# Optimization experiments

Hardware: AMD Instinct MI355X
Metric: run time of the kernel (lower is better)

## Reference

```python
import jax, jax.numpy as jnp
import numpy as np

S, B, E, H, M = 1024, 4, 1024, 16, 128  # seq, batch, embed, heads, model_dims (key width)
V = E // H                              # value_dims = 64
_WSCALE = 1.0 / np.sqrt(E)              # keep softmax logits O(1)


def _cplx(re, im):
    return jax.lax.complex(re, im)


def setup_inputs() -> dict:
    key = jax.random.key(0)
    ks = jax.random.split(key, 10)
    n = lambda k, shp: jax.random.normal(k, shp, dtype=jnp.float32)
    w = lambda k, shp: n(k, shp) * np.float32(_WSCALE / np.sqrt(2.0))
    return {
        "logits_re": n(ks[0], (S, B, E)),
        "logits_im": n(ks[1], (S, B, E)),
        "wq_re": w(ks[2], (H, M, E)), "wq_im": w(ks[3], (H, M, E)),
        "wk_re": w(ks[4], (H, M, E)), "wk_im": w(ks[5], (H, M, E)),
        "wv_re": w(ks[6], (H, V, E)), "wv_im": w(ks[7], (H, V, E)),
        "wo_re": w(ks[8], (E, E)),    "wo_im": w(ks[9], (E, E)),
    }


def reference(logits_re, logits_im, wq_re, wq_im, wk_re, wk_im,
              wv_re, wv_im, wo_re, wo_im):
    x = _cplx(logits_re, logits_im)          # (s, b, e) complex64
    wq = _cplx(wq_re, wq_im)                 # (h, m, e)
    wk = _cplx(wk_re, wk_im)
    wv = _cplx(wv_re, wv_im)                 # (h, v, e)
    wo = _cplx(wo_re, wo_im)                 # (e, e)

    q = jnp.einsum('hme,sbe->bhsm', wq, x)   # (b, h, s, m)
    k = jnp.einsum('hme,sbe->bhsm', wk, x)
    v = jnp.einsum('hve,sbe->bhsv', wv, x)   # (b, h, s, v)

    scores = jnp.einsum('bhsm,bhtm->bhst', q, k)         # complex, no conjugation (matches torch matmul)
    amp = jnp.abs(scores)                                # -> float32
    causal = jnp.triu(jnp.ones((S, S), dtype=bool), 1)   # True above diagonal -> masked
    amp = jnp.where(causal, -jnp.inf, amp) / jnp.sqrt(jnp.float32(M))
    attn = jax.nn.softmax(amp, axis=-1).astype(scores.dtype)  # cast back to complex64

    upd = jnp.einsum('bhst,bhtv->bhsv', attn, v)         # (b, h, s, v)
    upd = upd.transpose(2, 0, 1, 3).reshape(S, B, E)     # 's2 b (h v)'
    out = jnp.einsum('sbe,ef->sbf', upd, wo) + x         # residual
    # complex output returned as stacked (real, imag) float32 for harness compatibility
    return jnp.stack([out.real, out.imag])
```

## Files before the change

### kernel.cpp

```cpp
#include <hip/hip_runtime.h>
#include <math.h>

#define S_DIM 1024
#define B_DIM 4
#define E_DIM 1024
#define H_DIM 16
#define M_DIM 128
#define V_DIM 64

typedef __attribute__((ext_vector_type(8))) short short8;
typedef __attribute__((ext_vector_type(4))) float f32x4;
typedef __attribute__((ext_vector_type(4))) int int4v;

__device__ __forceinline__ unsigned short f2bf(float f) {
    union { float f; unsigned u; } v; v.f = f;
    unsigned r = v.u + 0x7FFFu + ((v.u >> 16) & 1u);
    return (unsigned short)(r >> 16);
}

__device__ __forceinline__ void async16(const unsigned short* g, unsigned short* l) {
    __builtin_amdgcn_global_load_lds(
        (const __attribute__((address_space(1))) void*)g,
        (__attribute__((address_space(3))) void*)l,
        16, 0, 0);
}

__global__ __launch_bounds__(256) void convert_pair(
    const float* __restrict__ re, const float* __restrict__ im,
    unsigned short* __restrict__ dre, unsigned short* __restrict__ dim_, int n4)
{
    int i = blockIdx.x * 256 + threadIdx.x;
    if (i >= n4) return;
    float4 r = ((const float4*)re)[i];
    float4 m = ((const float4*)im)[i];
    ushort4 ro, mo;
    ro.x = f2bf(r.x); ro.y = f2bf(r.y); ro.z = f2bf(r.z); ro.w = f2bf(r.w);
    mo.x = f2bf(m.x); mo.y = f2bf(m.y); mo.z = f2bf(m.z); mo.w = f2bf(m.w);
    ((ushort4*)dre)[i] = ro;
    ((ushort4*)dim_)[i] = mo;
}

__global__ __launch_bounds__(256) void transpose_wo(
    const float* __restrict__ wore, const float* __restrict__ woim,
    unsigned short* __restrict__ wtre, unsigned short* __restrict__ wtim)
{
    __shared__ float tr[32][33], ti[32][33];
    const int bx = blockIdx.x * 32;
    const int by = blockIdx.y * 32;
    const int tx = threadIdx.x & 31, ty = threadIdx.x >> 5;
    for (int i = ty; i < 32; i += 8) {
        tr[i][tx] = wore[(bx + i) * E_DIM + by + tx];
        ti[i][tx] = woim[(bx + i) * E_DIM + by + tx];
    }
    __syncthreads();
    for (int i = ty; i < 32; i += 8) {
        wtre[(by + i) * E_DIM + bx + tx] = f2bf(tr[tx][i]);
        wtim[(by + i) * E_DIM + bx + tx] = f2bf(ti[tx][i]);
    }
}

__global__ __launch_bounds__(256) void vtrans(
    const unsigned short* __restrict__ vrp, const unsigned short* __restrict__ vip,
    unsigned short* __restrict__ vrt, unsigned short* __restrict__ vit)
{
    __shared__ unsigned short tl[2][64][66];
    const int tid = threadIdx.x;
    const int t0 = blockIdx.x * 64;
    const int bh = blockIdx.y;
    #pragma unroll
    for (int pl = 0; pl < 2; ++pl) {
        const unsigned short* src = pl ? vip : vrp;
        #pragma unroll
        for (int p = 0; p < 2; ++p) {
            const int row = p * 32 + (tid >> 3);
            const int col = (tid & 7) * 8;
            short8 d = *(const short8*)&src[((size_t)bh * S_DIM + t0 + row) * V_DIM + col];
            #pragma unroll
            for (int j = 0; j < 8; ++j) tl[pl][row][col + j] = (unsigned short)d[j];
        }
    }
    __syncthreads();
    #pragma unroll
    for (int pl = 0; pl < 2; ++pl) {
        unsigned short* dst = pl ? vit : vrt;
        #pragma unroll
        for (int p = 0; p < 2; ++p) {
            const int v = p * 32 + (tid >> 3);
            const int tc = (tid & 7) * 8;
            short8 d;
            #pragma unroll
            for (int j = 0; j < 8; ++j) d[j] = (short)tl[pl][tc + j][v];
            *(short8*)&dst[((size_t)bh * V_DIM + v) * S_DIM + t0 + tc] = d;
        }
    }
}

template<int MODE>
__global__ __launch_bounds__(512, 2) void cgemm(
    const unsigned short* __restrict__ Are, const unsigned short* __restrict__ Aim,
    const unsigned short* __restrict__ Bre, const unsigned short* __restrict__ Bim,
    unsigned short* __restrict__ qrp, unsigned short* __restrict__ qip,
    unsigned short* __restrict__ krp, unsigned short* __restrict__ kip,
    unsigned short* __restrict__ vrp, unsigned short* __restrict__ vip,
    const float* __restrict__ xre, const float* __restrict__ xim,
    float* __restrict__ out)
{
    __shared__ __align__(16) unsigned short lds[65536];
    const int tid  = threadIdx.x;
    const int wave = tid >> 6;
    const int lane = tid & 63;
    const int r0 = blockIdx.x * 128;
    const int j0 = blockIdx.y * 128;
    const int wm = (wave >> 2) * 64;
    const int wn = (wave & 3) * 32;

    f32x4 accre[4][2], accim[4][2];
    #pragma unroll
    for (int i = 0; i < 4; ++i)
        #pragma unroll
        for (int j = 0; j < 2; ++j) {
            accre[i][j] = (f32x4){0.f, 0.f, 0.f, 0.f};
            accim[i][j] = (f32x4){0.f, 0.f, 0.f, 0.f};
        }

    const int fr = lane & 15;
    const int xc = ((lane >> 4) ^ ((lane >> 1) & 3)) * 8;

    const int srow = tid >> 2;
    const int scol = ((tid & 3) ^ ((tid >> 3) & 3)) * 8;

    #define STAGE(sl) { \
        const int col_ = (sl) * 32 + scol; \
        unsigned short* d_ = &lds[(((sl) & 3) << 14) + tid * 8]; \
        async16(Are + (size_t)(r0 + srow) * E_DIM + col_, d_); \
        async16(Aim + (size_t)(r0 + srow) * E_DIM + col_, d_ + 4096); \
        async16(Bre + (size_t)(j0 + srow) * E_DIM + col_, d_ + 8192); \
        async16(Bim + (size_t)(j0 + srow) * E_DIM + col_, d_ + 12288); }

    STAGE(0) STAGE(1) STAGE(2)
    asm volatile("s_waitcnt vmcnt(8)" ::: "memory");
    __builtin_amdgcn_s_barrier();

    #pragma unroll 1
    for (int s = 0; s < 32; ++s) {
        if (s < 29) STAGE(s + 3)

        const unsigned short* buf = &lds[(s & 3) << 14];
        short8 ar[4], ai[4], brr[2], bii[2];
        #pragma unroll
        for (int im = 0; im < 4; ++im) {
            const int ro = (wm + im * 16 + fr) * 32 + xc;
            ar[im] = *(const short8*)&buf[ro];
            ai[im] = *(const short8*)&buf[4096 + ro];
        }
        #pragma unroll
        for (int jn = 0; jn < 2; ++jn) {
            const int ro = (wn + jn * 16 + fr) * 32 + xc;
            brr[jn] = *(const short8*)&buf[8192 + ro];
            bii[jn] = *(const short8*)&buf[12288 + ro];
        }

        if (s < 29)       { asm volatile("s_waitcnt vmcnt(8)" ::: "memory"); }
        else if (s == 29) { asm volatile("s_waitcnt vmcnt(4)" ::: "memory"); }
        else              { asm volatile("s_waitcnt vmcnt(0)" ::: "memory"); }
        __builtin_amdgcn_s_barrier();
        asm volatile("s_waitcnt lgkmcnt(0)" ::: "memory");
        __builtin_amdgcn_sched_barrier(0);

        __builtin_amdgcn_s_setprio(1);
        #pragma unroll
        for (int jn = 0; jn < 2; ++jn) {
            int4v t = *(int4v*)&bii[jn];
            t = t ^ (int)0x80008000;
            const short8 bin = *(short8*)&t;
            #pragma unroll
            for (int im = 0; im < 4; ++im) {
                accre[im][jn] = __builtin_amdgcn_mfma_f32_16x16x32_bf16(ar[im], brr[jn], accre[im][jn], 0, 0, 0);
                accre[im][jn] = __builtin_amdgcn_mfma_f32_16x16x32_bf16(ai[im], bin,     accre[im][jn], 0, 0, 0);
                accim[im][jn] = __builtin_amdgcn_mfma_f32_16x16x32_bf16(ar[im], bii[jn], accim[im][jn], 0, 0, 0);
                accim[im][jn] = __builtin_amdgcn_mfma_f32_16x16x32_bf16(ai[im], brr[jn], accim[im][jn], 0, 0, 0);
            }
        }
        __builtin_amdgcn_s_setprio(0);
        __builtin_amdgcn_s_barrier();
    }
    #undef STAGE

    #pragma unroll
    for (int im = 0; im < 4; ++im) {
        #pragma unroll
        for (int reg = 0; reg < 4; ++reg) {
            const int r = r0 + wm + im * 16 + (lane >> 4) * 4 + reg;
            #pragma unroll
            for (int jn = 0; jn < 2; ++jn) {
                const int j = j0 + wn + jn * 16 + fr;
                const float vr = accre[im][jn][reg];
                const float vi = accim[im][jn][reg];
                if (MODE == 0) {
                    const int s = r >> 2, b = r & 3;
                    if (j < 2048) {
                        const int h = j >> 7, m = j & 127;
                        const size_t off = ((size_t)(b * H_DIM + h) * S_DIM + s) * M_DIM + m;
                        qrp[off] = f2bf(vr); qip[off] = f2bf(vi);
                    } else if (j < 4096) {
                        const int jl = j - 2048, h = jl >> 7, m = jl & 127;
                        const size_t off = ((size_t)(b * H_DIM + h) * S_DIM + s) * M_DIM + m;
                        krp[off] = f2bf(vr); kip[off] = f2bf(vi);
                    } else {
                        const int jl = j - 4096, h = jl >> 6, vv = jl & 63;
                        const size_t off = ((size_t)(b * H_DIM + h) * S_DIM + s) * V_DIM + vv;
                        vrp[off] = f2bf(vr); vip[off] = f2bf(vi);
                    }
                } else {
                    const int idx = r * E_DIM + j;
                    out[idx] = vr + xre[idx];
                    out[S_DIM * B_DIM * E_DIM + idx] = vi + xim[idx];
                }
            }
        }
    }
}

__global__ __launch_bounds__(256, 2) void attn_mfma(
    const unsigned short* __restrict__ qr, const unsigned short* __restrict__ qi,
    const unsigned short* __restrict__ kr, const unsigned short* __restrict__ ki,
    const unsigned short* __restrict__ vrt, const unsigned short* __restrict__ vit,
    unsigned short* __restrict__ updre, unsigned short* __restrict__ updim)
{
    __shared__ __align__(16) unsigned short Ks[2][64][136];
    __shared__ __align__(16) unsigned short Vs[2][64][72];
    __shared__ __align__(16) unsigned short Ps[4][16][80];

    const int tid  = threadIdx.x;
    const int wave = tid >> 6;
    const int lane = tid & 63;
    const int qt = (int)gridDim.x - 1 - blockIdx.x;
    const int bh = blockIdx.y;
    const int q0 = qt * 64;
    const size_t base_qk = (size_t)bh * S_DIM * M_DIM;
    const size_t base_v  = (size_t)bh * V_DIM * S_DIM;

    const int fr = lane & 15;
    const int fg = lane >> 4;
    const int fk = fg * 8;

    const int krow = tid >> 4, kcol = (tid & 15) * 8;
    const int vrow = tid >> 3, vcol = (tid & 7) * 8;

    #pragma unroll
    for (int pl = 0; pl < 2; ++pl) {
        const unsigned short* src = pl ? qi : qr;
        #pragma unroll
        for (int p = 0; p < 4; ++p)
            *(short8*)&Ks[pl][p * 16 + krow][kcol] =
                *(const short8*)&src[base_qk + (size_t)(q0 + p * 16 + krow) * M_DIM + kcol];
    }
    __syncthreads();
    short8 Bqr[4], Bqi[4];
    {
        const int qrow = wave * 16 + fr;
        #pragma unroll
        for (int ks = 0; ks < 4; ++ks) {
            Bqr[ks] = *(const short8*)&Ks[0][qrow][ks * 32 + fk];
            Bqi[ks] = *(const short8*)&Ks[1][qrow][ks * 32 + fk];
        }
    }

    f32x4 Ore[4], Oim[4];
    #pragma unroll
    for (int vt = 0; vt < 4; ++vt) {
        Ore[vt] = (f32x4){0.f, 0.f, 0.f, 0.f};
        Oim[vt] = (f32x4){0.f, 0.f, 0.f, 0.f};
    }
    float mrun = -INFINITY, lrun = 0.f;

    const float scale = 0.088388347648318447f;
    const int qglob = q0 + wave * 16 + fr;

    short8 pk[2][4], pv[2][2];
    #pragma unroll
    for (int pl = 0; pl < 2; ++pl) {
        const unsigned short* src = pl ? ki : kr;
        #pragma unroll
        for (int p = 0; p < 4; ++p)
            pk[pl][p] = *(const short8*)&src[base_qk + (size_t)(p * 16 + krow) * M_DIM + kcol];
    }
    #pragma unroll
    for (int pl = 0; pl < 2; ++pl) {
        const unsigned short* src = pl ? vit : vrt;
        #pragma unroll
        for (int p = 0; p < 2; ++p)
            pv[pl][p] = *(const short8*)&src[base_v + (size_t)(p * 32 + vrow) * S_DIM + vcol];
    }

    for (int t0 = 0; t0 <= q0; t0 += 64) {
        __syncthreads();
        #pragma unroll
        for (int pl = 0; pl < 2; ++pl) {
            #pragma unroll
            for (int p = 0; p < 4; ++p)
                *(short8*)&Ks[pl][p * 16 + krow][kcol] = pk[pl][p];
            #pragma unroll
            for (int p = 0; p < 2; ++p)
                *(short8*)&Vs[pl][p * 32 + vrow][vcol] = pv[pl][p];
        }
        __syncthreads();

        if (t0 + 64 <= q0) {
            const int tn = t0 + 64;
            #pragma unroll
            for (int pl = 0; pl < 2; ++pl) {
                const unsigned short* src = pl ? ki : kr;
                #pragma unroll
                for (int p = 0; p < 4; ++p)
                    pk[pl][p] = *(const short8*)&src[base_qk + (size_t)(tn + p * 16 + krow) * M_DIM + kcol];
            }
            #pragma unroll
            for (int pl = 0; pl < 2; ++pl) {
                const unsigned short* src = pl ? vit : vrt;
                #pragma unroll
                for (int p = 0; p < 2; ++p)
                    pv[pl][p] = *(const short8*)&src[base_v + (size_t)(p * 32 + vrow) * S_DIM + tn + vcol];
            }
        }

        f32x4 Sre[4], Sim[4];
        #pragma unroll
        for (int tt = 0; tt < 4; ++tt) {
            Sre[tt] = (f32x4){0.f, 0.f, 0.f, 0.f};
            Sim[tt] = (f32x4){0.f, 0.f, 0.f, 0.f};
            const int trow = tt * 16 + fr;
            #pragma unroll
            for (int ks = 0; ks < 4; ++ks) {
                const short8 Akr = *(const short8*)&Ks[0][trow][ks * 32 + fk];
                const short8 Aki = *(const short8*)&Ks[1][trow][ks * 32 + fk];
                int4v t = *(int4v*)&Aki;
                t = t ^ (int)0x80008000;
                const short8 Akin = *(short8*)&t;
                Sre[tt] = __builtin_amdgcn_mfma_f32_16x16x32_bf16(Akr,  Bqr[ks], Sre[tt], 0, 0, 0);
                Sre[tt] = __builtin_amdgcn_mfma_f32_16x16x32_bf16(Akin, Bqi[ks], Sre[tt], 0, 0, 0);
                Sim[tt] = __builtin_amdgcn_mfma_f32_16x16x32_bf16(Akr,  Bqi[ks], Sim[tt], 0, 0, 0);
                Sim[tt] = __builtin_amdgcn_mfma_f32_16x16x32_bf16(Aki,  Bqr[ks], Sim[tt], 0, 0, 0);
            }
        }

        float amp[4][4];
        float rowmax = -INFINITY;
        #pragma unroll
        for (int tt = 0; tt < 4; ++tt) {
            #pragma unroll
            for (int r = 0; r < 4; ++r) {
                const int tg = t0 + tt * 16 + fg * 4 + r;
                const float re = Sre[tt][r], im = Sim[tt][r];
                const float a = sqrtf(re * re + im * im) * scale;
                const float av = (tg > qglob) ? -INFINITY : a;
                amp[tt][r] = av;
                rowmax = fmaxf(rowmax, av);
            }
        }
        rowmax = fmaxf(rowmax, __shfl_xor(rowmax, 16));
        rowmax = fmaxf(rowmax, __shfl_xor(rowmax, 32));
        const float nm = fmaxf(mrun, rowmax);
        const float alpha = __expf(mrun - nm);
        mrun = nm;
        float psum = 0.f;
        #pragma unroll
        for (int tt = 0; tt < 4; ++tt) {
            #pragma unroll
            for (int r = 0; r < 4; ++r) {
                const float p = __expf(amp[tt][r] - nm);
                psum += p;
                Ps[wave][fr][tt * 16 + fg * 4 + r] = f2bf(p);
            }
        }
        psum += __shfl_xor(psum, 16);
        psum += __shfl_xor(psum, 32);
        lrun = lrun * alpha + psum;

        #pragma unroll
        for (int vt = 0; vt < 4; ++vt)
            #pragma unroll
            for (int r = 0; r < 4; ++r) { Ore[vt][r] *= alpha; Oim[vt][r] *= alpha; }

        const short8 Bp0 = *(const short8*)&Ps[wave][fr][fk];
        const short8 Bp1 = *(const short8*)&Ps[wave][fr][32 + fk];
        #pragma unroll
        for (int vt = 0; vt < 4; ++vt) {
            const int vr2 = vt * 16 + fr;
            const short8 Ar0 = *(const short8*)&Vs[0][vr2][fk];
            const short8 Ar1 = *(const short8*)&Vs[0][vr2][32 + fk];
            const short8 Ai0 = *(const short8*)&Vs[1][vr2][fk];
            const short8 Ai1 = *(const short8*)&Vs[1][vr2][32 + fk];
            Ore[vt] = __builtin_amdgcn_mfma_f32_16x16x32_bf16(Ar0, Bp0, Ore[vt], 0, 0, 0);
            Ore[vt] = __builtin_amdgcn_mfma_f32_16x16x32_bf16(Ar1, Bp1, Ore[vt], 0, 0, 0);
            Oim[vt] = __builtin_amdgcn_mfma_f32_16x16x32_bf16(Ai0, Bp0, Oim[vt], 0, 0, 0);
            Oim[vt] = __builtin_amdgcn_mfma_f32_16x16x32_bf16(Ai1, Bp1, Oim[vt], 0, 0, 0);
        }
    }

    const int b = bh >> 4, h = bh & 15;
    const float inv = 1.0f / lrun;
    const size_t base = ((size_t)(qglob * B_DIM + b)) * E_DIM + h * V_DIM;
    #pragma unroll
    for (int vt = 0; vt < 4; ++vt) {
        ushort4 pr, pi;
        pr.x = f2bf(Ore[vt][0] * inv); pr.y = f2bf(Ore[vt][1] * inv);
        pr.z = f2bf(Ore[vt][2] * inv); pr.w = f2bf(Ore[vt][3] * inv);
        pi.x = f2bf(Oim[vt][0] * inv); pi.y = f2bf(Oim[vt][1] * inv);
        pi.z = f2bf(Oim[vt][2] * inv); pi.w = f2bf(Oim[vt][3] * inv);
        *(ushort4*)&updre[base + vt * 16 + fg * 4] = pr;
        *(ushort4*)&updim[base + vt * 16 + fg * 4] = pi;
    }
}

extern "C" void kernel_launch(void* const* d_in, const int* in_sizes, int n_in,
                              void* d_out, int out_size, void* d_ws, size_t ws_size,
                              hipStream_t stream) {
    const float* xre  = (const float*)d_in[0];
    const float* xim  = (const float*)d_in[1];
    const float* wqre = (const float*)d_in[2];
    const float* wqim = (const float*)d_in[3];
    const float* wkre = (const float*)d_in[4];
    const float* wkim = (const float*)d_in[5];
    const float* wvre = (const float*)d_in[6];
    const float* wvim = (const float*)d_in[7];
    const float* wore = (const float*)d_in[8];
    const float* woim = (const float*)d_in[9];
    float* out = (float*)d_out;

    char* p = (char*)d_ws;
    const size_t QK = (size_t)B_DIM * H_DIM * S_DIM * M_DIM;
    const size_t VS = (size_t)B_DIM * H_DIM * S_DIM * V_DIM;
    const size_t SBE = (size_t)S_DIM * B_DIM * E_DIM;
    unsigned short* qrw = (unsigned short*)p;  p += QK * 2;
    unsigned short* qiw = (unsigned short*)p;  p += QK * 2;
    unsigned short* krw = (unsigned short*)p;  p += QK * 2;
    unsigned short* kiw = (unsigned short*)p;  p += QK * 2;
    unsigned short* vrw = (unsigned short*)p;  p += VS * 2;
    unsigned short* viw = (unsigned short*)p;  p += VS * 2;
    unsigned short* vrt = (unsigned short*)p;  p += VS * 2;
    unsigned short* vit = (unsigned short*)p;  p += VS * 2;
    unsigned short* updre = (unsigned short*)p; p += SBE * 2;
    unsigned short* updim = (unsigned short*)p; p += SBE * 2;
    unsigned short* xbre  = (unsigned short*)p; p += SBE * 2;
    unsigned short* xbim  = (unsigned short*)p; p += SBE * 2;
    unsigned short* wbre  = (unsigned short*)p; p += (size_t)5120 * E_DIM * 2;
    unsigned short* wbim  = (unsigned short*)p; p += (size_t)5120 * E_DIM * 2;
    unsigned short* wtre  = (unsigned short*)p; p += (size_t)E_DIM * E_DIM * 2;
    unsigned short* wtim  = (unsigned short*)p; p += (size_t)E_DIM * E_DIM * 2;

    convert_pair<<<4096, 256, 0, stream>>>(xre, xim, xbre, xbim, 1048576);
    convert_pair<<<2048, 256, 0, stream>>>(wqre, wqim, wbre, wbim, 524288);
    convert_pair<<<2048, 256, 0, stream>>>(wkre, wkim, wbre + 2048*1024, wbim + 2048*1024, 524288);
    convert_pair<<<1024, 256, 0, stream>>>(wvre, wvim, wbre + 4096*1024, wbim + 4096*1024, 262144);
    transpose_wo<<<dim3(32, 32), 256, 0, stream>>>(wore, woim, wtre, wtim);

    cgemm<0><<<dim3(32, 40), 512, 0, stream>>>(xbre, xbim, wbre, wbim,
                                               qrw, qiw, krw, kiw, vrw, viw,
                                               nullptr, nullptr, nullptr);
    vtrans<<<dim3(16, 64), 256, 0, stream>>>(vrw, viw, vrt, vit);
    attn_mfma<<<dim3(16, 64), 256, 0, stream>>>(qrw, qiw, krw, kiw, vrt, vit, updre, updim);
    cgemm<1><<<dim3(32, 8), 512, 0, stream>>>(updre, updim, wtre, wtim,
                                              nullptr, nullptr, nullptr, nullptr, nullptr, nullptr,
                                              xre, xim, out);
}
```

Before: 507.7 us.

## Shrink complex GEMM tiles to 128x64 with 4 waves and double buffering

The complex bf16 GEMM drops from 512-thread blocks with 128x128 tiles and a 4-stage async LDS pipeline to 256-thread blocks with 128x64 tiles and a 2-stage double buffer. The grid doubles and LDS use per block falls, so more blocks can be resident at once and the small output-projection GEMM fills more CUs. The cost is that each block reuses loaded data less, and the shallower prefetch with a full vmcnt(0) wait every iteration exposes more global-load latency.

```diff
diff --git a/kernel.cpp b/kernel.cpp
--- a/kernel.cpp
+++ b/kernel.cpp
@@ -96,7 +96,7 @@
 }
 
 template<int MODE>
-__global__ __launch_bounds__(512, 2) void cgemm(
+__global__ __launch_bounds__(256, 3) void cgemm(
     const unsigned short* __restrict__ Are, const unsigned short* __restrict__ Aim,
     const unsigned short* __restrict__ Bre, const unsigned short* __restrict__ Bim,
     unsigned short* __restrict__ qrp, unsigned short* __restrict__ qip,
@@ -105,14 +105,14 @@
     const float* __restrict__ xre, const float* __restrict__ xim,
     float* __restrict__ out)
 {
-    __shared__ __align__(16) unsigned short lds[65536];
+    __shared__ __align__(16) unsigned short lds[24576];
     const int tid  = threadIdx.x;
     const int wave = tid >> 6;
     const int lane = tid & 63;
     const int r0 = blockIdx.x * 128;
-    const int j0 = blockIdx.y * 128;
-    const int wm = (wave >> 2) * 64;
-    const int wn = (wave & 3) * 32;
+    const int j0 = blockIdx.y * 64;
+    const int wm = (wave >> 1) * 64;
+    const int wn = (wave & 1) * 32;
 
     f32x4 accre[4][2], accim[4][2];
     #pragma unroll
@@ -123,29 +123,38 @@
             accim[i][j] = (f32x4){0.f, 0.f, 0.f, 0.f};
         }
 
+    const int srow = lane >> 2;
+    const int scol = ((lane & 3) ^ ((lane >> 3) & 3)) * 8;
+
     const int fr = lane & 15;
     const int xc = ((lane >> 4) ^ ((lane >> 1) & 3)) * 8;
 
-    const int srow = tid >> 2;
-    const int scol = ((tid & 3) ^ ((tid >> 3) & 3)) * 8;
-
-    #define STAGE(sl) { \
-        const int col_ = (sl) * 32 + scol; \
-        unsigned short* d_ = &lds[(((sl) & 3) << 14) + tid * 8]; \
-        async16(Are + (size_t)(r0 + srow) * E_DIM + col_, d_); \
-        async16(Aim + (size_t)(r0 + srow) * E_DIM + col_, d_ + 4096); \
-        async16(Bre + (size_t)(j0 + srow) * E_DIM + col_, d_ + 8192); \
-        async16(Bim + (size_t)(j0 + srow) * E_DIM + col_, d_ + 12288); }
-
-    STAGE(0) STAGE(1) STAGE(2)
-    asm volatile("s_waitcnt vmcnt(8)" ::: "memory");
+    #define STAGE(sl, bb) { \
+        const int kg = (sl) * 32; \
+        unsigned short* b_ = &lds[(bb) * 12288]; \
+        _Pragma("unroll") \
+        for (int c = 0; c < 2; ++c) { \
+            const int row0 = wave * 32 + c * 16; \
+            const size_t g = (size_t)(r0 + row0 + srow) * E_DIM + kg + scol; \
+            async16(Are + g, b_ + row0 * 32); \
+            async16(Aim + g, b_ + 4096 + row0 * 32); \
+        } \
+        { \
+            const int row0 = wave * 16; \
+            const size_t g = (size_t)(j0 + row0 + srow) * E_DIM + kg + scol; \
+            async16(Bre + g, b_ + 8192 + row0 * 32); \
+            async16(Bim + g, b_ + 10240 + row0 * 32); \
+        } }
+
+    STAGE(0, 0)
+    asm volatile("s_waitcnt vmcnt(0)" ::: "memory");
     __builtin_amdgcn_s_barrier();
 
     #pragma unroll 1
     for (int s = 0; s < 32; ++s) {
-        if (s < 29) STAGE(s + 3)
-
-        const unsigned short* buf = &lds[(s & 3) << 14];
+        if (s < 31) STAGE(s + 1, (s + 1) & 1)
+
+        const unsigned short* buf = &lds[(s & 1) * 12288];
         short8 ar[4], ai[4], brr[2], bii[2];
         #pragma unroll
         for (int im = 0; im < 4; ++im) {
@@ -157,13 +166,8 @@
         for (int jn = 0; jn < 2; ++jn) {
             const int ro = (wn + jn * 16 + fr) * 32 + xc;
             brr[jn] = *(const short8*)&buf[8192 + ro];
-            bii[jn] = *(const short8*)&buf[12288 + ro];
-        }
-
-        if (s < 29)       { asm volatile("s_waitcnt vmcnt(8)" ::: "memory"); }
-        else if (s == 29) { asm volatile("s_waitcnt vmcnt(4)" ::: "memory"); }
-        else              { asm volatile("s_waitcnt vmcnt(0)" ::: "memory"); }
-        __builtin_amdgcn_s_barrier();
+            bii[jn] = *(const short8*)&buf[10240 + ro];
+        }
         asm volatile("s_waitcnt lgkmcnt(0)" ::: "memory");
         __builtin_amdgcn_sched_barrier(0);
 
@@ -182,7 +186,11 @@
             }
         }
         __builtin_amdgcn_s_setprio(0);
-        __builtin_amdgcn_s_barrier();
+
+        if (s < 31) {
+            asm volatile("s_waitcnt vmcnt(0)" ::: "memory");
+            __builtin_amdgcn_s_barrier();
+        }
     }
     #undef STAGE
 
@@ -455,12 +463,12 @@
     convert_pair<<<1024, 256, 0, stream>>>(wvre, wvim, wbre + 4096*1024, wbim + 4096*1024, 262144);
     transpose_wo<<<dim3(32, 32), 256, 0, stream>>>(wore, woim, wtre, wtim);
 
-    cgemm<0><<<dim3(32, 40), 512, 0, stream>>>(xbre, xbim, wbre, wbim,
+    cgemm<0><<<dim3(32, 80), 256, 0, stream>>>(xbre, xbim, wbre, wbim,
                                                qrw, qiw, krw, kiw, vrw, viw,
                                                nullptr, nullptr, nullptr);
     vtrans<<<dim3(16, 64), 256, 0, stream>>>(vrw, viw, vrt, vit);
     attn_mfma<<<dim3(16, 64), 256, 0, stream>>>(qrw, qiw, krw, kiw, vrt, vit, updre, updim);
-    cgemm<1><<<dim3(32, 8), 512, 0, stream>>>(updre, updim, wtre, wtim,
-                                              nullptr, nullptr, nullptr, nullptr, nullptr, nullptr,
-                                              xre, xim, out);
-}
+    cgemm<1><<<dim3(32, 16), 256, 0, stream>>>(updre, updim, wtre, wtim,
+                                               nullptr, nullptr, nullptr, nullptr, nullptr, nullptr,
+                                               xre, xim, out);
+}
```

After: 501.2 us. About the same (-1.3%).
